# Performance work log

Measured on AMD Instinct MI355X. Metric: run time of the kernel, lower is better.

The kernel has to match this reference:

```python
import jax, jax.numpy as jnp
import numpy as np

N = 8192       # nodes
IN_F = 512     # in_features
OUT_F = 256    # out_features


def setup_inputs() -> dict:
    key = jax.random.key(0)
    k1, k2, k3, k4 = jax.random.split(key, 4)
    # xavier_uniform-like scales for params
    w_scale = 1.414 * (6.0 / (IN_F + OUT_F)) ** 0.5
    a_scale = 1.414 * (6.0 / (2 * OUT_F + 1)) ** 0.5
    x = jax.random.normal(k1, (N, IN_F), jnp.float32)
    W = jax.random.uniform(k2, (IN_F, OUT_F), jnp.float32, -w_scale, w_scale)
    a = jax.random.uniform(k3, (2 * OUT_F, 1), jnp.float32, -a_scale, a_scale)
    adj = jax.random.randint(k4, (N, N), 0, 2, jnp.int32)
    return {"x": x, "W": W, "a": a, "adj": adj}


def reference(x, W, a, adj):
    # h = x @ W : [N, OUT_F]
    h = x @ W
    f = W.shape[1]
    a1, a2 = a[:f], a[f:]          # each [OUT_F, 1]
    # Original builds a_input[i,j] = concat(h_i, h_j) then matmuls with a.
    # Equivalent decomposition: e[i,j] = h_i . a1 + h_j . a2
    e = (h @ a1) + (h @ a2).T      # [N, N]
    neg = jnp.float32(-9e15)
    attention = jnp.where(adj > 0, e, neg)   # no softmax in the original
    h_prime = attention @ h        # [N, OUT_F]
    return h_prime
```

## Files before the change

### kernel.cpp

```cpp
#include <hip/hip_runtime.h>


#define NEG_BIG (-9000000000000000.0f)
#define POS_BIG (9000000000000000.0f)

typedef __bf16 bf16x8 __attribute__((ext_vector_type(8)));
typedef float f32x16 __attribute__((ext_vector_type(16)));

static __device__ __forceinline__ unsigned short f2bf(float f) {
  unsigned u = __builtin_bit_cast(unsigned, f);
  u = u + 0x7FFFu + ((u >> 16) & 1u);
  return (unsigned short)(u >> 16);
}
static __device__ __forceinline__ float bfbits2f(unsigned hi16) {
  return __builtin_bit_cast(float, hi16 << 16);
}
static __device__ __forceinline__ unsigned pk2(float a, float b) {
  return (unsigned)f2bf(a) | ((unsigned)f2bf(b) << 16);
}
static __device__ __forceinline__ unsigned m2(int a, int b) {
  return (unsigned)(a + (b << 16)) * 0x3F80u;
}
static __device__ __forceinline__ bf16x8 asbf(int4 q) {
  return __builtin_bit_cast(bf16x8, q);
}
static __device__ __forceinline__ f32x16 mfma(bf16x8 a, int4 b, f32x16 c) {
  return __builtin_amdgcn_mfma_f32_32x32x16_bf16(a, asbf(b), c, 0, 0, 0);
}

__global__ void k1a_wt(const float* __restrict__ W, unsigned short* __restrict__ WT,
                       float* __restrict__ T) {
  const int i = blockIdx.x * 256 + threadIdx.x;
  const int k = i >> 8, n = i & 255;
  WT[n * 512 + k] = f2bf(W[i]);
  if (blockIdx.x == 0) T[threadIdx.x] = 0.f;
}

__global__ __launch_bounds__(256) void k1b_h(const float* __restrict__ x,
    const unsigned short* __restrict__ WT, unsigned short* __restrict__ hP) {
  __shared__ unsigned short XS[64 * 264];
  const int t = threadIdx.x;
  const int mt = blockIdx.x;
  const int m0 = mt << 5;
  const int row = t >> 3, c7 = t & 7;
  const float* xr = x + (size_t)(m0 + row) * 512 + c7 * 4;
  const int gb = c7 >> 1, off = (t & 1) * 4;
#pragma unroll
  for (int j = 0; j < 16; ++j) {
    float4 v = *(const float4*)(xr + 32 * j);
    *(uint2*)&XS[(gb + 4 * j) * 264 + row * 8 + off] =
        make_uint2(pk2(v.x, v.y), pk2(v.z, v.w));
  }
  __syncthreads();
  const int w = t >> 6, l = t & 63, l31 = l & 31, lh = l >> 5;
  f32x16 acc0, acc1;
  for (int i = 0; i < 16; ++i) { acc0[i] = 0.f; acc1[i] = 0.f; }
  const int nt0 = w * 2;
  const unsigned short* w0 = WT + (size_t)(nt0 * 32 + l31) * 512 + lh * 8;
  const unsigned short* w1 = w0 + 32 * 512;
  const char* XB = (const char*)XS + lh * 528 + l31 * 16;
#pragma unroll 4
  for (int ks = 0; ks < 32; ++ks) {
    bf16x8 Af = *(const bf16x8*)(XB + ks * 1056);
    int4 b0 = *(const int4*)(w0 + ks * 16);
    int4 b1 = *(const int4*)(w1 + ks * 16);
    acc0 = mfma(Af, b0, acc0);
    acc1 = mfma(Af, b1, acc1);
  }
#pragma unroll
  for (int reg = 0; reg < 16; ++reg) {
    const int mm = (reg & 3) + 8 * (reg >> 2) + 4 * lh;
    hP[(size_t)mt * 8192 + (nt0 * 32 + l31) * 32 + mm] = f2bf(acc0[reg]);
    hP[(size_t)mt * 8192 + ((nt0 + 1) * 32 + l31) * 32 + mm] = f2bf(acc1[reg]);
  }
}

__global__ __launch_bounds__(256) void k2_colsum(const unsigned short* __restrict__ hP,
                                                 float* __restrict__ T) {
  const int t = threadIdx.x;
  const int b = blockIdx.x;
  const int4* p = (const int4*)(hP + (size_t)b * 8192 + t * 32);
  int4 q0 = p[0], q1 = p[1], q2 = p[2], q3 = p[3];
  float s = 0.f;
  const unsigned* u0 = (const unsigned*)&q0;
  const unsigned* u1 = (const unsigned*)&q1;
  const unsigned* u2 = (const unsigned*)&q2;
  const unsigned* u3 = (const unsigned*)&q3;
#pragma unroll
  for (int i = 0; i < 4; ++i) {
    s += bfbits2f(u0[i] & 0xFFFFu) + bfbits2f(u0[i] >> 16);
    s += bfbits2f(u1[i] & 0xFFFFu) + bfbits2f(u1[i] >> 16);
    s += bfbits2f(u2[i] & 0xFFFFu) + bfbits2f(u2[i] >> 16);
    s += bfbits2f(u3[i] & 0xFFFFu) + bfbits2f(u3[i] >> 16);
  }
  atomicAdd(&T[t], s);
}

__global__ void k2b_init(const float* __restrict__ T, float* __restrict__ out) {
  const int i = blockIdx.x * 256 + threadIdx.x;
  const int n4 = (i & 63) * 4;
  float4 tv = *(const float4*)(T + n4);
  float4 o;
  o.x = NEG_BIG * tv.x; o.y = NEG_BIG * tv.y;
  o.z = NEG_BIG * tv.z; o.w = NEG_BIG * tv.w;
  ((float4*)out)[i] = o;
}

template<int MODE>
__global__ __launch_bounds__(256, 2) void k3_att(const int* __restrict__ adj,
    const unsigned short* __restrict__ hP, float* __restrict__ outp) {
  __shared__ unsigned short S[4][2][4 * 512];
  const int t = threadIdx.x, blk = blockIdx.x;
  const int s = blk & 7;
  const int rg = blk >> 3;
  const int w = t >> 6, l = t & 63, l31 = l & 31, lh = l >> 5;
  const int rt = rg * 2 + (w >> 1);
  const int nh = w & 1;

  const int* aB = adj + (size_t)(rt * 64 + (l >> 3)) * 8192 + s * 1024 + (l & 7) * 4;
  const int woff = ((l & 7) >> 1) * 512 + (l >> 3) * 8 + (l & 1) * 4;
  unsigned short* const Sw0 = &S[w][0][0];
  unsigned short* const Sw1 = &S[w][1][0];
  const unsigned short* hB = hP + (size_t)(s * 32) * 8192
                              + (size_t)(nh * 128 + l31) * 32 + lh * 8;
  const int fr = lh * 1024 + l31 * 16;

  f32x16 acc[2][4];
#pragma unroll
  for (int mt = 0; mt < 2; ++mt)
#pragma unroll
    for (int nt = 0; nt < 4; ++nt)
#pragma unroll
      for (int i = 0; i < 16; ++i) acc[mt][nt][i] = 0.f;

  int4 gA[8], Bv[8];

#define ALOAD(it)                                                           \
  _Pragma("unroll")                                                         \
  for (int q = 0; q < 8; ++q)                                               \
    gA[q] = *(const int4*)(aB + (size_t)q * 8 * 8192 + (it) * 32);
#define APACK(buf)                                                          \
  _Pragma("unroll")                                                         \
  for (int q = 0; q < 8; ++q)                                               \
    *(uint2*)&buf[woff + q * 64] =                                          \
        make_uint2(m2(gA[q].x, gA[q].y), m2(gA[q].z, gA[q].w));
#define BLOAD(it)                                                           \
  {                                                                         \
    const unsigned short* hb = hB + (size_t)(it) * 8192;                    \
    _Pragma("unroll")                                                       \
    for (int ks = 0; ks < 2; ++ks)                                          \
      _Pragma("unroll")                                                     \
      for (int nt = 0; nt < 4; ++nt)                                        \
        Bv[ks * 4 + nt] = *(const int4*)(hb + nt * 1024 + ks * 16);         \
  }
#define COMP(buf)                                                           \
  {                                                                         \
    const char* Ab = (const char*)(buf) + fr;                               \
    _Pragma("unroll")                                                       \
    for (int ks = 0; ks < 2; ++ks) {                                        \
      bf16x8 A0 = *(const bf16x8*)(Ab + ks * 2048);                         \
      bf16x8 A1 = *(const bf16x8*)(Ab + ks * 2048 + 512);                   \
      _Pragma("unroll")                                                     \
      for (int nt = 0; nt < 4; ++nt) {                                      \
        acc[0][nt] = mfma(A0, Bv[ks * 4 + nt], acc[0][nt]);                 \
        acc[1][nt] = mfma(A1, Bv[ks * 4 + nt], acc[1][nt]);                 \
      }                                                                     \
    }                                                                       \
  }

  ALOAD(0)
  APACK(Sw0)
  ALOAD(1)

#pragma unroll 1
  for (int it = 0; it < 32; ++it) {
    unsigned short* const Scur = (it & 1) ? Sw1 : Sw0;
    unsigned short* const Snxt = (it & 1) ? Sw0 : Sw1;
    BLOAD(it)
    if (it + 1 < 32) { APACK(Snxt) }
    if (it + 2 < 32) { ALOAD(it + 2) }
    COMP(Scur)
  }
#undef ALOAD
#undef APACK
#undef BLOAD
#undef COMP

#pragma unroll
  for (int mt = 0; mt < 2; ++mt)
#pragma unroll
    for (int nt = 0; nt < 4; ++nt) {
      const int nn = nh * 128 + nt * 32 + l31;
#pragma unroll
      for (int reg = 0; reg < 16; ++reg) {
        const int rr = rt * 64 + mt * 32 + (reg & 3) + 8 * (reg >> 2) + 4 * lh;
        if (MODE == 0) {
          outp[(size_t)s * 2097152 + (size_t)rr * 256 + nn] = acc[mt][nt][reg];
        } else {
          atomicAdd(outp + (size_t)rr * 256 + nn, POS_BIG * acc[mt][nt][reg]);
        }
      }
    }
}

__global__ __launch_bounds__(256) void k4_reduce(const float* __restrict__ P,
    const float* __restrict__ T, float* __restrict__ out) {
  const int i = blockIdx.x * 256 + threadIdx.x;
  float4 tv = *(const float4*)(T + (i & 63) * 4);
  const float4* P4 = (const float4*)P;
  float sx = 0.f, sy = 0.f, sz = 0.f, sw = 0.f;
#pragma unroll
  for (int sp = 0; sp < 8; ++sp) {
    float4 v = P4[(size_t)sp * 524288 + i];
    sx += v.x; sy += v.y; sz += v.z; sw += v.w;
  }
  float4 o;
  o.x = POS_BIG * sx + NEG_BIG * tv.x;
  o.y = POS_BIG * sy + NEG_BIG * tv.y;
  o.z = POS_BIG * sz + NEG_BIG * tv.z;
  o.w = POS_BIG * sw + NEG_BIG * tv.w;
  ((float4*)out)[i] = o;
}

extern "C" void kernel_launch(void* const* d_in, const int* in_sizes, int n_in,
                              void* d_out, int out_size, void* d_ws, size_t ws_size,
                              hipStream_t stream) {
  const float* x = (const float*)d_in[0];
  const float* W = (const float*)d_in[1];
  const int* adj = (const int*)d_in[3];
  float* out = (float*)d_out;
  char* ws = (char*)d_ws;
  unsigned short* WT = (unsigned short*)(ws);
  unsigned short* hP = (unsigned short*)(ws + (1 << 20));
  float* T = (float*)(ws + (6 << 20));
  float* P = (float*)(ws + (8 << 20));

  const bool fit = ws_size >= ((size_t)(8 << 20) + (size_t)64 * 1024 * 1024);

  k1a_wt<<<512, 256, 0, stream>>>(W, WT, T);
  k1b_h<<<256, 256, 0, stream>>>(x, WT, hP);
  k2_colsum<<<256, 256, 0, stream>>>(hP, T);
  if (fit) {
    k3_att<0><<<512, 256, 0, stream>>>(adj, hP, P);
    k4_reduce<<<2048, 256, 0, stream>>>(P, T, out);
  } else {
    k2b_init<<<2048, 256, 0, stream>>>(T, out);
    k3_att<1><<<512, 256, 0, stream>>>(adj, hP, out);
  }
}
```

Before: 461.8 us.

## Drop split-K partials and compute full K per block with direct output

Replaces the 8-way split over adjacency columns, with its workspace partials and separate reduce kernel, by a single kernel where each 256-thread block owns 32 rows and all 256 output columns and loops over the full 8192 K range. The loop is unrolled into a four-stage software pipeline with deeper adjacency prefetch, and the epilogue writes the final scaled value directly. This removes the 64 MB partial write/read and one launch. The cost is only 256 blocks, so fewer waves per CU are available to hide latency, and each block runs a much longer serial loop.

```diff
diff --git a/kernel.cpp b/kernel.cpp
--- a/kernel.cpp
+++ b/kernel.cpp
@@ -2,7 +2,6 @@
 
 
 #define NEG_BIG (-9000000000000000.0f)
-#define POS_BIG (9000000000000000.0f)
 
 typedef __bf16 bf16x8 __attribute__((ext_vector_type(8)));
 typedef float f32x16 __attribute__((ext_vector_type(16)));
@@ -96,130 +95,105 @@
   atomicAdd(&T[t], s);
 }
 
-__global__ void k2b_init(const float* __restrict__ T, float* __restrict__ out) {
-  const int i = blockIdx.x * 256 + threadIdx.x;
-  const int n4 = (i & 63) * 4;
-  float4 tv = *(const float4*)(T + n4);
-  float4 o;
-  o.x = NEG_BIG * tv.x; o.y = NEG_BIG * tv.y;
-  o.z = NEG_BIG * tv.z; o.w = NEG_BIG * tv.w;
-  ((float4*)out)[i] = o;
-}
-
-template<int MODE>
-__global__ __launch_bounds__(256, 2) void k3_att(const int* __restrict__ adj,
-    const unsigned short* __restrict__ hP, float* __restrict__ outp) {
-  __shared__ unsigned short S[4][2][4 * 512];
+__global__ __launch_bounds__(256) void k3_att(const int* __restrict__ adj,
+    const unsigned short* __restrict__ hP, const float* __restrict__ T,
+    float* __restrict__ out) {
+  __shared__ unsigned short S[4][2][1024];
   const int t = threadIdx.x, blk = blockIdx.x;
-  const int s = blk & 7;
-  const int rg = blk >> 3;
   const int w = t >> 6, l = t & 63, l31 = l & 31, lh = l >> 5;
-  const int rt = rg * 2 + (w >> 1);
-  const int nh = w & 1;
-
-  const int* aB = adj + (size_t)(rt * 64 + (l >> 3)) * 8192 + s * 1024 + (l & 7) * 4;
-  const int woff = ((l & 7) >> 1) * 512 + (l >> 3) * 8 + (l & 1) * 4;
+  const int r0 = blk * 32;
+
+  const int* aB = adj + (size_t)(r0 + (l >> 3)) * 8192 + (l & 7) * 4;
+  const int woff = ((l & 7) >> 1) * 256 + (l >> 3) * 8 + (l & 1) * 4;
+  const unsigned short* hB = hP + (size_t)(w * 64 + l31) * 32 + lh * 8;
+  const int fr = lh * 512 + l31 * 16;
   unsigned short* const Sw0 = &S[w][0][0];
   unsigned short* const Sw1 = &S[w][1][0];
-  const unsigned short* hB = hP + (size_t)(s * 32) * 8192
-                              + (size_t)(nh * 128 + l31) * 32 + lh * 8;
-  const int fr = lh * 1024 + l31 * 16;
-
-  f32x16 acc[2][4];
-#pragma unroll
-  for (int mt = 0; mt < 2; ++mt)
-#pragma unroll
-    for (int nt = 0; nt < 4; ++nt)
-#pragma unroll
-      for (int i = 0; i < 16; ++i) acc[mt][nt][i] = 0.f;
-
-  int4 gA[8], Bv[8];
-
-#define ALOAD(it)                                                           \
+
+  f32x16 acc0, acc1;
+#pragma unroll
+  for (int i = 0; i < 16; ++i) { acc0[i] = 0.f; acc1[i] = 0.f; }
+
+  int4 gA0[4], gA1[4], gA2[4], gA3[4], BvA[4], BvB[4];
+
+#define ALOAD(it, g)                                                        \
   _Pragma("unroll")                                                         \
-  for (int q = 0; q < 8; ++q)                                               \
-    gA[q] = *(const int4*)(aB + (size_t)q * 8 * 8192 + (it) * 32);
-#define APACK(buf)                                                          \
+  for (int q = 0; q < 4; ++q)                                               \
+    g[q] = *(const int4*)(aB + (size_t)q * 65536 + (it) * 32);
+#define APACK(buf, g)                                                       \
   _Pragma("unroll")                                                         \
-  for (int q = 0; q < 8; ++q)                                               \
+  for (int q = 0; q < 4; ++q)                                               \
     *(uint2*)&buf[woff + q * 64] =                                          \
-        make_uint2(m2(gA[q].x, gA[q].y), m2(gA[q].z, gA[q].w));
-#define BLOAD(it)                                                           \
+        make_uint2(m2(g[q].x, g[q].y), m2(g[q].z, g[q].w));
+#define BLOAD(it, Bv)                                                       \
   {                                                                         \
     const unsigned short* hb = hB + (size_t)(it) * 8192;                    \
-    _Pragma("unroll")                                                       \
-    for (int ks = 0; ks < 2; ++ks)                                          \
-      _Pragma("unroll")                                                     \
-      for (int nt = 0; nt < 4; ++nt)                                        \
-        Bv[ks * 4 + nt] = *(const int4*)(hb + nt * 1024 + ks * 16);         \
-  }
-#define COMP(buf)                                                           \
+    Bv[0] = *(const int4*)(hb);                                             \
+    Bv[1] = *(const int4*)(hb + 1024);                                      \
+    Bv[2] = *(const int4*)(hb + 16);                                        \
+    Bv[3] = *(const int4*)(hb + 1024 + 16);                                 \
+  }
+#define COMP(buf, Bv)                                                       \
   {                                                                         \
     const char* Ab = (const char*)(buf) + fr;                               \
-    _Pragma("unroll")                                                       \
-    for (int ks = 0; ks < 2; ++ks) {                                        \
-      bf16x8 A0 = *(const bf16x8*)(Ab + ks * 2048);                         \
-      bf16x8 A1 = *(const bf16x8*)(Ab + ks * 2048 + 512);                   \
-      _Pragma("unroll")                                                     \
-      for (int nt = 0; nt < 4; ++nt) {                                      \
-        acc[0][nt] = mfma(A0, Bv[ks * 4 + nt], acc[0][nt]);                 \
-        acc[1][nt] = mfma(A1, Bv[ks * 4 + nt], acc[1][nt]);                 \
-      }                                                                     \
-    }                                                                       \
-  }
-
-  ALOAD(0)
-  APACK(Sw0)
-  ALOAD(1)
+    bf16x8 A0_ = *(const bf16x8*)(Ab);                                      \
+    bf16x8 A1_ = *(const bf16x8*)(Ab + 1024);                               \
+    acc0 = mfma(A0_, Bv[0], acc0);                                          \
+    acc1 = mfma(A0_, Bv[1], acc1);                                          \
+    acc0 = mfma(A1_, Bv[2], acc0);                                          \
+    acc1 = mfma(A1_, Bv[3], acc1);                                          \
+  }
+
+  ALOAD(0, gA0)
+  APACK(Sw0, gA0)
+  ALOAD(1, gA1)
+  ALOAD(2, gA2)
+  BLOAD(0, BvA)
 
 #pragma unroll 1
-  for (int it = 0; it < 32; ++it) {
-    unsigned short* const Scur = (it & 1) ? Sw1 : Sw0;
-    unsigned short* const Snxt = (it & 1) ? Sw0 : Sw1;
-    BLOAD(it)
-    if (it + 1 < 32) { APACK(Snxt) }
-    if (it + 2 < 32) { ALOAD(it + 2) }
-    COMP(Scur)
+  for (int it = 0; it < 256; it += 4) {
+    BLOAD(it + 1, BvB)
+    APACK(Sw1, gA1)
+    if (it + 3 < 256) { ALOAD(it + 3, gA3) }
+    COMP(Sw0, BvA)
+
+    if (it + 2 < 256) { BLOAD(it + 2, BvA) }
+    if (it + 2 < 256) { APACK(Sw0, gA2) }
+    if (it + 4 < 256) { ALOAD(it + 4, gA0) }
+    COMP(Sw1, BvB)
+
+    if (it + 3 < 256) { BLOAD(it + 3, BvB) }
+    if (it + 3 < 256) { APACK(Sw1, gA3) }
+    if (it + 5 < 256) { ALOAD(it + 5, gA1) }
+    if (it + 2 < 256) { COMP(Sw0, BvA) }
+
+    if (it + 4 < 256) { BLOAD(it + 4, BvA) }
+    if (it + 4 < 256) { APACK(Sw0, gA0) }
+    if (it + 6 < 256) { ALOAD(it + 6, gA2) }
+    if (it + 3 < 256) { COMP(Sw1, BvB) }
   }
 #undef ALOAD
 #undef APACK
 #undef BLOAD
 #undef COMP
 
-#pragma unroll
-  for (int mt = 0; mt < 2; ++mt)
-#pragma unroll
-    for (int nt = 0; nt < 4; ++nt) {
-      const int nn = nh * 128 + nt * 32 + l31;
-#pragma unroll
-      for (int reg = 0; reg < 16; ++reg) {
-        const int rr = rt * 64 + mt * 32 + (reg & 3) + 8 * (reg >> 2) + 4 * lh;
-        if (MODE == 0) {
-          outp[(size_t)s * 2097152 + (size_t)rr * 256 + nn] = acc[mt][nt][reg];
-        } else {
-          atomicAdd(outp + (size_t)rr * 256 + nn, POS_BIG * acc[mt][nt][reg]);
-        }
-      }
+  const int cb = w * 64 + l31;
+  {
+    const float tv = T[cb];
+#pragma unroll
+    for (int reg = 0; reg < 16; ++reg) {
+      const int rr = r0 + (reg & 3) + 8 * (reg >> 2) + 4 * lh;
+      out[(size_t)rr * 256 + cb] = NEG_BIG * (tv - acc0[reg]);
     }
-}
-
-__global__ __launch_bounds__(256) void k4_reduce(const float* __restrict__ P,
-    const float* __restrict__ T, float* __restrict__ out) {
-  const int i = blockIdx.x * 256 + threadIdx.x;
-  float4 tv = *(const float4*)(T + (i & 63) * 4);
-  const float4* P4 = (const float4*)P;
-  float sx = 0.f, sy = 0.f, sz = 0.f, sw = 0.f;
-#pragma unroll
-  for (int sp = 0; sp < 8; ++sp) {
-    float4 v = P4[(size_t)sp * 524288 + i];
-    sx += v.x; sy += v.y; sz += v.z; sw += v.w;
-  }
-  float4 o;
-  o.x = POS_BIG * sx + NEG_BIG * tv.x;
-  o.y = POS_BIG * sy + NEG_BIG * tv.y;
-  o.z = POS_BIG * sz + NEG_BIG * tv.z;
-  o.w = POS_BIG * sw + NEG_BIG * tv.w;
-  ((float4*)out)[i] = o;
+  }
+  {
+    const float tv = T[cb + 32];
+#pragma unroll
+    for (int reg = 0; reg < 16; ++reg) {
+      const int rr = r0 + (reg & 3) + 8 * (reg >> 2) + 4 * lh;
+      out[(size_t)rr * 256 + cb + 32] = NEG_BIG * (tv - acc1[reg]);
+    }
+  }
 }
 
 extern "C" void kernel_launch(void* const* d_in, const int* in_sizes, int n_in,
@@ -233,18 +207,9 @@
   unsigned short* WT = (unsigned short*)(ws);
   unsigned short* hP = (unsigned short*)(ws + (1 << 20));
   float* T = (float*)(ws + (6 << 20));
-  float* P = (float*)(ws + (8 << 20));
-
-  const bool fit = ws_size >= ((size_t)(8 << 20) + (size_t)64 * 1024 * 1024);
 
   k1a_wt<<<512, 256, 0, stream>>>(W, WT, T);
   k1b_h<<<256, 256, 0, stream>>>(x, WT, hP);
   k2_colsum<<<256, 256, 0, stream>>>(hP, T);
-  if (fit) {
-    k3_att<0><<<512, 256, 0, stream>>>(adj, hP, P);
-    k4_reduce<<<2048, 256, 0, stream>>>(P, T, out);
-  } else {
-    k2b_init<<<2048, 256, 0, stream>>>(T, out);
-    k3_att<1><<<512, 256, 0, stream>>>(adj, hP, out);
-  }
-}
+  k3_att<<<256, 256, 0, stream>>>(adj, hP, T, out);
+}
```

New measurement: 490.6 us. +6.2%, slower.
